# Kernel optimization log

Measured on AMD Instinct MI355X. Metric: run time of the kernel, lower is better.

The kernel has to match this reference:

```python
import jax, jax.numpy as jnp
import numpy as np
from jax import lax

NUM_GROUPS = 16
GN_EPS = 1e-5
POOL = 4
CLAMP_MIN, CLAMP_MAX = 0.0, 1.0


def setup_inputs() -> dict:
    key = jax.random.key(0)
    ks = jax.random.split(key, 4)
    x = jax.random.normal(ks[0], (128, 8, 128, 128), dtype=jnp.float32)
    conv_weight = jax.random.normal(ks[1], (64, 8, 3, 3), dtype=jnp.float32) * 0.1
    conv_bias = jax.random.normal(ks[2], (64,), dtype=jnp.float32) * 0.1
    gn_weight = jnp.ones((64,), dtype=jnp.float32)
    gn_bias = jnp.zeros((64,), dtype=jnp.float32)
    scale = jax.random.normal(ks[3], (64, 1, 1), dtype=jnp.float32)
    return {"x": x, "conv_weight": conv_weight, "conv_bias": conv_bias,
            "gn_weight": gn_weight, "gn_bias": gn_bias, "scale": scale}


def reference(x, conv_weight, conv_bias, gn_weight, gn_bias, scale):
    # Conv2d (stride=1, padding=0)
    y = lax.conv_general_dilated(
        x, conv_weight, window_strides=(1, 1), padding='VALID',
        dimension_numbers=('NCHW', 'OIHW', 'NCHW'))
    y = y + conv_bias[None, :, None, None]  # [B, C, H, W] = [128, 64, 126, 126]

    # GroupNorm over (channels-in-group, H, W) per sample
    B, C, H, W = y.shape
    yg = y.reshape(B, NUM_GROUPS, C // NUM_GROUPS, H, W)
    mean = jnp.mean(yg, axis=(2, 3, 4), keepdims=True)
    var = jnp.var(yg, axis=(2, 3, 4), keepdims=True)
    yn = ((yg - mean) * lax.rsqrt(var + GN_EPS)).reshape(B, C, H, W)
    yn = yn * gn_weight[None, :, None, None] + gn_bias[None, :, None, None]

    # scale (broadcast [C,1,1])
    yn = yn * scale[None]

    # MaxPool2d(kernel=4, stride=4)
    p = lax.reduce_window(yn, -jnp.inf, lax.max,
                          window_dimensions=(1, 1, POOL, POOL),
                          window_strides=(1, 1, POOL, POOL),
                          padding='VALID')  # [128, 64, 31, 31]

    # clamp
    return jnp.clip(p, CLAMP_MIN, CLAMP_MAX)
```

## Files before the change

kernel.cpp:

```cpp
#include <hip/hip_runtime.h>
#include <math.h>

typedef _Float16 f16x8 __attribute__((ext_vector_type(8)));
typedef float f32x4 __attribute__((ext_vector_type(4)));

#define CIN 8
#define HIN 128
#define WIN 128
#define OH 126
#define OW 126
#define COUT 64
#define NB 128
#define NGROUPS 16
#define CPG 4
#define PWN 31
#define XROWS 34

#define NPOOL (NB*PWN*PWN*COUT)
#define OFF_PART (NPOOL/2)
#define NPART (NB*NGROUPS*16*2)

__global__ __launch_bounds__(256, 2)
void conv_mfma_kernel(const float* __restrict__ x,
                      const float* __restrict__ w,
                      const float* __restrict__ bias,
                      const float* __restrict__ gnw,
                      const float* __restrict__ scale,
                      float* __restrict__ ws)
{
  __shared__ __align__(16) _Float16 xs[XROWS*34*8];
  __shared__ __align__(16) _Float16 wls[9*64*8];
  __shared__ float red[4][16][2];

  const int tid  = threadIdx.x;
  const int lane = tid & 63, wave = tid >> 6;
  const int tileIdx = blockIdx.x;
  const int tx = tileIdx & 3, ty = tileIdx >> 2;
  const int b  = blockIdx.y;
  const int ox0 = tx*32, oy0 = ty*32;

  for (int idx = tid; idx < 9*64*8; idx += 256) {
    const int ci = idx & 7, n = (idx >> 3) & 63, khw = idx >> 9;
    wls[idx] = (_Float16)w[(n*CIN + ci)*9 + khw];
  }

  const float* xb = x + (size_t)b * CIN*HIN*WIN;
  for (int p = tid; p < XROWS*34; p += 256) {
    const int r = p / 34, c = p - r*34;
    const int iy = oy0 + r, ix = ox0 + c;
    const bool ok = (iy < HIN) && (ix < WIN);
    const int gbase = iy*WIN + ix;
    f16x8 pk;
    #pragma unroll
    for (int ci = 0; ci < 8; ++ci) {
      const float v = ok ? xb[ci*HIN*WIN + gbase] : 0.f;
      pk[ci] = (_Float16)v;
    }
    *(f16x8*)&xs[p*8] = pk;
  }
  __syncthreads();

  const int q = lane >> 4, ln = lane & 15;

  f16x8 bf[4][3];
  #pragma unroll
  for (int nt = 0; nt < 4; ++nt) {
    #pragma unroll
    for (int c = 0; c < 2; ++c)
      bf[nt][c] = *(const f16x8*)&wls[((c*4 + q)*64 + nt*16 + ln)*8];
    if (q == 0)
      bf[nt][2] = *(const f16x8*)&wls[((8)*64 + nt*16 + ln)*8];
    else
      bf[nt][2] = (f16x8){0,0,0,0,0,0,0,0};
  }

  const int dy = ln >> 2, dx = ln & 3;
  int aoff[3];
  #pragma unroll
  for (int c = 0; c < 3; ++c) {
    const int khw = c*4 + q;
    const int ky = khw / 3, kx = khw - 3*(khw/3);
    aoff[c] = (khw < 9) ? ((dy + ky)*34 + (dx + kx))*8 : 0;
  }

  float bias_r[4], sgn[4];
  #pragma unroll
  for (int nt = 0; nt < 4; ++nt) {
    const int c = nt*16 + ln;
    bias_r[nt] = bias[c];
    sgn[nt] = (gnw[c]*scale[c] >= 0.f) ? 1.f : -1.f;
  }

  float s[4]  = {0.f,0.f,0.f,0.f};
  float sq[4] = {0.f,0.f,0.f,0.f};
  _Float16* wext = (_Float16*)ws;

  #pragma unroll 2
  for (int i = 0; i < 16; ++i) {
    const int wyl = wave*2 + (i >> 3), wxl = i & 7;
    const int base = (wyl*4*34 + wxl*4)*8;

    f32x4 acc[4];
    #pragma unroll
    for (int nt = 0; nt < 4; ++nt) {
      const float bv = bias_r[nt];
      acc[nt] = (f32x4){bv, bv, bv, bv};
    }
    #pragma unroll
    for (int c = 0; c < 3; ++c) {
      const f16x8 a = *(const f16x8*)&xs[base + aoff[c]];
      #pragma unroll
      for (int nt = 0; nt < 4; ++nt)
        acc[nt] = __builtin_amdgcn_mfma_f32_16x16x32_f16(a, bf[nt][c], acc[nt], 0, 0, 0);
    }

    const int wyg = ty*8 + wyl, wxg = tx*8 + wxl;
    if ((wyg < PWN) && (wxg < PWN)) {
      const size_t rowbase = ((size_t)(b*PWN + wyg)*PWN + wxg)*COUT;
      float m4[4];
      #pragma unroll
      for (int nt = 0; nt < 4; ++nt) {
        const float v0 = acc[nt][0], v1 = acc[nt][1];
        const float v2 = acc[nt][2], v3 = acc[nt][3];
        s[nt]  += (v0+v1) + (v2+v3);
        sq[nt] += v0*v0 + v1*v1 + v2*v2 + v3*v3;
        const float sg = sgn[nt];
        float m = fmaxf(fmaxf(sg*v0, sg*v1), fmaxf(sg*v2, sg*v3));
        m = fmaxf(m, __shfl_xor(m, 16, 64));
        m = fmaxf(m, __shfl_xor(m, 32, 64));
        m4[nt] = sg*m;
      }
      float mv = m4[0];
      mv = (q == 1) ? m4[1] : mv;
      mv = (q == 2) ? m4[2] : mv;
      mv = (q == 3) ? m4[3] : mv;
      wext[rowbase + lane] = (_Float16)mv;
    } else {
      const bool yv = (wyg*4 + q) < OH;
      #pragma unroll
      for (int nt = 0; nt < 4; ++nt) {
        #pragma unroll
        for (int r = 0; r < 4; ++r) {
          const bool okp = yv && (wxg*4 + r < OW);
          const float v = okp ? acc[nt][r] : 0.f;
          s[nt] += v; sq[nt] += v*v;
        }
      }
    }
  }

  #pragma unroll
  for (int nt = 0; nt < 4; ++nt) {
    float a = s[nt], c2 = sq[nt];
    a  += __shfl_xor(a, 16, 64);  a  += __shfl_xor(a, 32, 64);
    a  += __shfl_xor(a, 1, 64);   a  += __shfl_xor(a, 2, 64);
    c2 += __shfl_xor(c2, 16, 64); c2 += __shfl_xor(c2, 32, 64);
    c2 += __shfl_xor(c2, 1, 64);  c2 += __shfl_xor(c2, 2, 64);
    if (lane < 16 && (lane & 3) == 0) {
      red[wave][nt*4 + (ln >> 2)][0] = a;
      red[wave][nt*4 + (ln >> 2)][1] = c2;
    }
  }
  __syncthreads();
  if (tid < 32) {
    const int g = tid >> 1, k = tid & 1;
    const float t = red[0][g][k] + red[1][g][k] + red[2][g][k] + red[3][g][k];
    ws[OFF_PART + (((size_t)b*NGROUPS + g)*16 + tileIdx)*2 + k] = t;
  }
}

__global__ __launch_bounds__(256)
void tail_kernel(const float* __restrict__ gnw,
                 const float* __restrict__ gnb,
                 const float* __restrict__ scale,
                 const float* __restrict__ ws,
                 float* __restrict__ out)
{
  __shared__ float stat[NGROUPS*2];
  __shared__ float AB[128];
  __shared__ float vout[COUT*PWN];

  const int tid = threadIdx.x;
  const int xb  = blockIdx.x;
  const int b   = blockIdx.y;

  if (tid < 32) {
    const int g = tid >> 1, k = tid & 1;
    const float* p = ws + OFF_PART + (size_t)(b*NGROUPS + g)*32 + k;
    float a = 0.f;
    #pragma unroll
    for (int t = 0; t < 16; ++t) a += p[t*2];
    stat[g*2 + k] = a;
  }
  __syncthreads();
  if (tid < COUT) {
    const int c = tid, g = c >> 2;
    const float N = (float)(CPG * OH * OW);
    const float mean = stat[g*2] / N;
    const float var  = stat[g*2 + 1] / N - mean*mean;
    const float inv  = rsqrtf(var + 1e-5f);
    const float ag   = inv * gnw[c];
    AB[c]      = ag * scale[c];
    AB[64 + c] = (gnb[c] - mean * ag) * scale[c];
  }
  __syncthreads();

  const _Float16* wext = (const _Float16*)ws;
  #pragma unroll
  for (int r = 0; r < 2; ++r) {
    const int wy = xb*2 + r;
    if (wy >= PWN) break;
    const size_t rb = (size_t)(b*PWN + wy)*PWN*COUT;

    if (tid < 248) {
      const f16x8 e = *(const f16x8*)&wext[rb + tid*8];
      const int wx = tid >> 3, c0 = (tid & 7)*8;
      #pragma unroll
      for (int j = 0; j < 8; ++j) {
        const int c = c0 + j;
        float v = fmaf(AB[c], (float)e[j], AB[64 + c]);
        v = fminf(fmaxf(v, 0.f), 1.f);
        vout[c*PWN + wx] = v;
      }
    }
    __syncthreads();
    for (int e = tid; e < COUT*PWN; e += 256) {
      const int c = e / PWN, wx = e - c*PWN;
      out[(((size_t)b*COUT + c)*PWN + wy)*PWN + wx] = vout[e];
    }
    __syncthreads();
  }
}

extern "C" void kernel_launch(void* const* d_in, const int* in_sizes, int n_in,
                              void* d_out, int out_size, void* d_ws, size_t ws_size,
                              hipStream_t stream)
{
  const float* x     = (const float*)d_in[0];
  const float* cw    = (const float*)d_in[1];
  const float* cb    = (const float*)d_in[2];
  const float* gnw   = (const float*)d_in[3];
  const float* gnb   = (const float*)d_in[4];
  const float* scale = (const float*)d_in[5];
  float* out = (float*)d_out;
  float* ws  = (float*)d_ws;

  dim3 gridA(16, NB, 1);
  conv_mfma_kernel<<<gridA, 256, 0, stream>>>(x, cw, cb, gnw, scale, ws);

  dim3 gridT(16, NB, 1);
  tail_kernel<<<gridT, 256, 0, stream>>>(gnw, gnb, scale, ws, out);
}
```

Baseline: 184.5 us.

## Split output channels across wave pairs with 512-thread conv blocks

Doubles the conv block to 512 threads, with each pair of waves splitting the 64 output channels into two halves of 32. Each wave now issues half the MFMAs and holds half the accumulators and weight fragments, and the launch bounds request higher occupancy. The aim is to hide the latency of the shared-memory staging and MFMA work across more waves. In exchange, every wave repeats the same LDS A-operand reads and shuffle reductions for its half, and the group-stat reduction is reorganised to match.

```diff
diff --git a/kernel.cpp b/kernel.cpp
--- a/kernel.cpp
+++ b/kernel.cpp
@@ -20,7 +20,7 @@
 #define OFF_PART (NPOOL/2)
 #define NPART (NB*NGROUPS*16*2)
 
-__global__ __launch_bounds__(256, 2)
+__global__ __launch_bounds__(512, 8)
 void conv_mfma_kernel(const float* __restrict__ x,
                       const float* __restrict__ w,
                       const float* __restrict__ bias,
@@ -30,22 +30,24 @@
 {
   __shared__ __align__(16) _Float16 xs[XROWS*34*8];
   __shared__ __align__(16) _Float16 wls[9*64*8];
-  __shared__ float red[4][16][2];
+  __shared__ float red[8][8][2];
 
   const int tid  = threadIdx.x;
-  const int lane = tid & 63, wave = tid >> 6;
+  const int lane = tid & 63, wv = tid >> 6;
+  const int h    = wv & 1;
+  const int wset = wv >> 1;
   const int tileIdx = blockIdx.x;
   const int tx = tileIdx & 3, ty = tileIdx >> 2;
   const int b  = blockIdx.y;
   const int ox0 = tx*32, oy0 = ty*32;
 
-  for (int idx = tid; idx < 9*64*8; idx += 256) {
+  for (int idx = tid; idx < 9*64*8; idx += 512) {
     const int ci = idx & 7, n = (idx >> 3) & 63, khw = idx >> 9;
     wls[idx] = (_Float16)w[(n*CIN + ci)*9 + khw];
   }
 
   const float* xb = x + (size_t)b * CIN*HIN*WIN;
-  for (int p = tid; p < XROWS*34; p += 256) {
+  for (int p = tid; p < XROWS*34; p += 512) {
     const int r = p / 34, c = p - r*34;
     const int iy = oy0 + r, ix = ox0 + c;
     const bool ok = (iy < HIN) && (ix < WIN);
@@ -61,15 +63,16 @@
   __syncthreads();
 
   const int q = lane >> 4, ln = lane & 15;
-
-  f16x8 bf[4][3];
-  #pragma unroll
-  for (int nt = 0; nt < 4; ++nt) {
+  const int cb = h*32;
+
+  f16x8 bf[2][3];
+  #pragma unroll
+  for (int nt = 0; nt < 2; ++nt) {
     #pragma unroll
     for (int c = 0; c < 2; ++c)
-      bf[nt][c] = *(const f16x8*)&wls[((c*4 + q)*64 + nt*16 + ln)*8];
+      bf[nt][c] = *(const f16x8*)&wls[((c*4 + q)*64 + cb + nt*16 + ln)*8];
     if (q == 0)
-      bf[nt][2] = *(const f16x8*)&wls[((8)*64 + nt*16 + ln)*8];
+      bf[nt][2] = *(const f16x8*)&wls[((8)*64 + cb + nt*16 + ln)*8];
     else
       bf[nt][2] = (f16x8){0,0,0,0,0,0,0,0};
   }
@@ -83,26 +86,26 @@
     aoff[c] = (khw < 9) ? ((dy + ky)*34 + (dx + kx))*8 : 0;
   }
 
-  float bias_r[4], sgn[4];
-  #pragma unroll
-  for (int nt = 0; nt < 4; ++nt) {
-    const int c = nt*16 + ln;
+  float bias_r[2], sgn[2];
+  #pragma unroll
+  for (int nt = 0; nt < 2; ++nt) {
+    const int c = cb + nt*16 + ln;
     bias_r[nt] = bias[c];
     sgn[nt] = (gnw[c]*scale[c] >= 0.f) ? 1.f : -1.f;
   }
 
-  float s[4]  = {0.f,0.f,0.f,0.f};
-  float sq[4] = {0.f,0.f,0.f,0.f};
+  float s[2]  = {0.f,0.f};
+  float sq[2] = {0.f,0.f};
   _Float16* wext = (_Float16*)ws;
 
   #pragma unroll 2
   for (int i = 0; i < 16; ++i) {
-    const int wyl = wave*2 + (i >> 3), wxl = i & 7;
+    const int wyl = wset*2 + (i >> 3), wxl = i & 7;
     const int base = (wyl*4*34 + wxl*4)*8;
 
-    f32x4 acc[4];
-    #pragma unroll
-    for (int nt = 0; nt < 4; ++nt) {
+    f32x4 acc[2];
+    #pragma unroll
+    for (int nt = 0; nt < 2; ++nt) {
       const float bv = bias_r[nt];
       acc[nt] = (f32x4){bv, bv, bv, bv};
     }
@@ -110,16 +113,16 @@
     for (int c = 0; c < 3; ++c) {
       const f16x8 a = *(const f16x8*)&xs[base + aoff[c]];
       #pragma unroll
-      for (int nt = 0; nt < 4; ++nt)
+      for (int nt = 0; nt < 2; ++nt)
         acc[nt] = __builtin_amdgcn_mfma_f32_16x16x32_f16(a, bf[nt][c], acc[nt], 0, 0, 0);
     }
 
     const int wyg = ty*8 + wyl, wxg = tx*8 + wxl;
     if ((wyg < PWN) && (wxg < PWN)) {
       const size_t rowbase = ((size_t)(b*PWN + wyg)*PWN + wxg)*COUT;
-      float m4[4];
-      #pragma unroll
-      for (int nt = 0; nt < 4; ++nt) {
+      float m4[2];
+      #pragma unroll
+      for (int nt = 0; nt < 2; ++nt) {
         const float v0 = acc[nt][0], v1 = acc[nt][1];
         const float v2 = acc[nt][2], v3 = acc[nt][3];
         s[nt]  += (v0+v1) + (v2+v3);
@@ -130,15 +133,12 @@
         m = fmaxf(m, __shfl_xor(m, 32, 64));
         m4[nt] = sg*m;
       }
-      float mv = m4[0];
-      mv = (q == 1) ? m4[1] : mv;
-      mv = (q == 2) ? m4[2] : mv;
-      mv = (q == 3) ? m4[3] : mv;
-      wext[rowbase + lane] = (_Float16)mv;
+      if (q < 2)
+        wext[rowbase + cb + lane] = (_Float16)(q ? m4[1] : m4[0]);
     } else {
       const bool yv = (wyg*4 + q) < OH;
       #pragma unroll
-      for (int nt = 0; nt < 4; ++nt) {
+      for (int nt = 0; nt < 2; ++nt) {
         #pragma unroll
         for (int r = 0; r < 4; ++r) {
           const bool okp = yv && (wxg*4 + r < OW);
@@ -150,21 +150,23 @@
   }
 
   #pragma unroll
-  for (int nt = 0; nt < 4; ++nt) {
+  for (int nt = 0; nt < 2; ++nt) {
     float a = s[nt], c2 = sq[nt];
     a  += __shfl_xor(a, 16, 64);  a  += __shfl_xor(a, 32, 64);
     a  += __shfl_xor(a, 1, 64);   a  += __shfl_xor(a, 2, 64);
     c2 += __shfl_xor(c2, 16, 64); c2 += __shfl_xor(c2, 32, 64);
     c2 += __shfl_xor(c2, 1, 64);  c2 += __shfl_xor(c2, 2, 64);
     if (lane < 16 && (lane & 3) == 0) {
-      red[wave][nt*4 + (ln >> 2)][0] = a;
-      red[wave][nt*4 + (ln >> 2)][1] = c2;
+      red[wv][nt*4 + (ln >> 2)][0] = a;
+      red[wv][nt*4 + (ln >> 2)][1] = c2;
     }
   }
   __syncthreads();
   if (tid < 32) {
     const int g = tid >> 1, k = tid & 1;
-    const float t = red[0][g][k] + red[1][g][k] + red[2][g][k] + red[3][g][k];
+    const int hg = g >> 3, gl = g & 7;
+    const float t = red[hg][gl][k] + red[hg+2][gl][k]
+                  + red[hg+4][gl][k] + red[hg+6][gl][k];
     ws[OFF_PART + (((size_t)b*NGROUPS + g)*16 + tileIdx)*2 + k] = t;
   }
 }
@@ -246,7 +248,7 @@
   float* ws  = (float*)d_ws;
 
   dim3 gridA(16, NB, 1);
-  conv_mfma_kernel<<<gridA, 256, 0, stream>>>(x, cw, cb, gnw, scale, ws);
+  conv_mfma_kernel<<<gridA, 512, 0, stream>>>(x, cw, cb, gnw, scale, ws);
 
   dim3 gridT(16, NB, 1);
   tail_kernel<<<gridT, 256, 0, stream>>>(gnw, gnb, scale, ws, out);
```

Measured after the change: 193.6 us. 4.9% more time.
